# Optimization experiments

Hardware: AMD Instinct MI355X
Metric: run time of the kernel (lower is better)

Reference implementation:

```python
import jax, jax.numpy as jnp
import numpy as np

B, T, C, H = 8, 2048, 1024, 64  # batch, seq (block_size), n_embd, head_size


def setup_inputs() -> dict:
    key = jax.random.key(0)
    kx, kq, kk, kv = jax.random.split(key, 4)
    s = 1.0 / np.sqrt(C)
    return {
        "x": jax.random.normal(kx, (B, T, C), dtype=jnp.float32),
        "Wq": jax.random.normal(kq, (C, H), dtype=jnp.float32) * s,
        "Wk": jax.random.normal(kk, (C, H), dtype=jnp.float32) * s,
        "Wv": jax.random.normal(kv, (C, H), dtype=jnp.float32) * s,
    }


def reference(x, Wq, Wk, Wv):
    t = x.shape[1]
    q = jnp.einsum("btc,ch->bth", x, Wq)
    k = jnp.einsum("btc,ch->bth", x, Wk)
    v = jnp.einsum("btc,ch->bth", x, Wv)
    scores = jnp.einsum("bqh,bkh->bqk", q, k) / jnp.sqrt(jnp.float32(H))
    causal = jnp.tril(jnp.ones((t, t), dtype=bool))  # tril mask
    scores = jnp.where(causal, scores, -jnp.inf)
    attn = jax.nn.softmax(scores, axis=-1)
    return jnp.einsum("bqk,bkh->bqh", attn, v)
```

## Files before the change

### kernel.cpp

```cpp
#include <hip/hip_runtime.h>
#include <hip/hip_bf16.h>

#define BB 8
#define TT 2048
#define CC 1024
#define HH 64
#define NSPLIT 8

typedef __attribute__((ext_vector_type(8)))  short bf16x8;
typedef __attribute__((ext_vector_type(4)))  float f32x4;
typedef __attribute__((ext_vector_type(16))) float f32x16;
typedef __attribute__((ext_vector_type(8)))  unsigned short us8;
typedef __attribute__((ext_vector_type(4)))  unsigned short us4;
typedef unsigned int u32;

static __device__ __forceinline__ unsigned short f2bf(float f) {
    union { float f; unsigned int u; } v; v.f = f;
    unsigned int u = v.u;
    return (unsigned short)((u + 0x7FFFu + ((u >> 16) & 1u)) >> 16);
}
static __device__ __forceinline__ float bf2f(unsigned short s) {
    union { u32 u; float f; } v; v.u = ((u32)s) << 16; return v.f;
}

__global__ __launch_bounds__(256) void prep_weights(
        const float* __restrict__ Wq, const float* __restrict__ Wk,
        const float* __restrict__ Wv, unsigned short* __restrict__ Wt) {
    __shared__ float tile[64][65];
    int w  = blockIdx.x >> 4;
    int c0 = (blockIdx.x & 15) * 64;
    const float* W = (w == 0) ? Wq : (w == 1) ? Wk : Wv;
    int li = threadIdx.x;
    {
        int c = li >> 2, h4 = (li & 3) * 16;
        const float* src = W + (size_t)(c0 + c) * HH + h4;
        #pragma unroll
        for (int i = 0; i < 4; ++i) {
            float4 v4 = *(const float4*)(src + i * 4);
            tile[c][h4 + i*4 + 0] = v4.x; tile[c][h4 + i*4 + 1] = v4.y;
            tile[c][h4 + i*4 + 2] = v4.z; tile[c][h4 + i*4 + 3] = v4.w;
        }
    }
    __syncthreads();
    float scale = (w == 0) ? 0.1803368802f : 1.0f;
    int h = li >> 2, cg = (li & 3) * 16;
    unsigned short* dst = Wt + (size_t)w * HH * CC + (size_t)h * CC + c0 + cg;
    #pragma unroll
    for (int i = 0; i < 16; ++i) dst[i] = f2bf(tile[cg + i][h] * scale);
}

__global__ __launch_bounds__(512, 4) void proj_qkv(
        const float* __restrict__ x, const unsigned short* __restrict__ Wt,
        unsigned short* __restrict__ qws, unsigned short* __restrict__ kws,
        unsigned short* __restrict__ vws) {
    __shared__ unsigned short Xs[2][64 * 64];
    __shared__ unsigned short Ws[2][192 * 64];
    int tid = threadIdx.x;
    int wv = tid >> 6, lane = tid & 63;
    int quad = (lane >> 4) & 3, lq = lane & 15;
    int mg = wv >> 2, ng = wv & 3;
    int r0 = blockIdx.x * 64;

    int xr = tid >> 3, xg = tid & 7;
    const float* xsrc = x + (size_t)(r0 + xr) * CC + xg * 8;
    int xdst = xr * 64 + ((xg ^ (xr & 7)) * 8);
    float4 xa[2], xb[2];

    f32x4 acc[2][3];
    #pragma unroll
    for (int mt = 0; mt < 2; ++mt)
        #pragma unroll
        for (int nt = 0; nt < 3; ++nt)
            #pragma unroll
            for (int i = 0; i < 4; ++i) acc[mt][nt][i] = 0.0f;

    auto stageW = [&](int buf, int kc) {
        #pragma unroll
        for (int i = 0; i < 3; ++i) {
            int fp = tid + i * 512;
            int r = fp >> 3, pb = fp & 7, g = pb ^ (r & 7);
            const u32 __attribute__((address_space(1)))* gsrc =
                (const u32 __attribute__((address_space(1)))*)
                    (Wt + (size_t)r * CC + kc * 64 + g * 8);
            u32 __attribute__((address_space(3)))* ldst =
                (u32 __attribute__((address_space(3)))*)(&Ws[buf][fp * 8]);
            __builtin_amdgcn_global_load_lds(gsrc, ldst, 16, 0, 0);
        }
    };
    auto loadX = [&](int set, int kc) {
        xa[set] = *(const float4*)(xsrc + kc * 64);
        xb[set] = *(const float4*)(xsrc + kc * 64 + 4);
    };
    auto writeX = [&](int set, int buf) {
        unsigned short h[8];
        h[0]=f2bf(xa[set].x); h[1]=f2bf(xa[set].y);
        h[2]=f2bf(xa[set].z); h[3]=f2bf(xa[set].w);
        h[4]=f2bf(xb[set].x); h[5]=f2bf(xb[set].y);
        h[6]=f2bf(xb[set].z); h[7]=f2bf(xb[set].w);
        *(us8*)&Xs[buf][xdst] = *(const us8*)h;
    };

    stageW(0, 0);
    loadX(0, 0); loadX(1, 1);
    writeX(0, 0);

    for (int kc = 0; kc < 16; ++kc) {
        int cur = kc & 1;
        if (kc < 15) asm volatile("s_waitcnt vmcnt(2) lgkmcnt(0)" ::: "memory");
        else         asm volatile("s_waitcnt vmcnt(0) lgkmcnt(0)" ::: "memory");
        __builtin_amdgcn_sched_barrier(0);
        __builtin_amdgcn_s_barrier();
        if (kc < 15) stageW(1 - cur, kc + 1);
        if (kc < 14) loadX(kc & 1, kc + 2);
        #pragma unroll
        for (int ks = 0; ks < 2; ++ks) {
            int g = ks * 4 + quad;
            bf16x8 a[2], b[3];
            #pragma unroll
            for (int mt = 0; mt < 2; ++mt) {
                int arow = mg * 32 + mt * 16 + lq;
                a[mt] = *(const bf16x8*)&Xs[cur][arow * 64 + (g ^ (lq & 7)) * 8];
            }
            #pragma unroll
            for (int nt = 0; nt < 3; ++nt) {
                int brow = ng * 48 + nt * 16 + lq;
                b[nt] = *(const bf16x8*)&Ws[cur][brow * 64 + (g ^ (lq & 7)) * 8];
            }
            #pragma unroll
            for (int mt = 0; mt < 2; ++mt)
                #pragma unroll
                for (int nt = 0; nt < 3; ++nt)
                    acc[mt][nt] = __builtin_amdgcn_mfma_f32_16x16x32_bf16(
                        a[mt], b[nt], acc[mt][nt], 0, 0, 0);
        }
        if (kc < 15) writeX((kc + 1) & 1, 1 - cur);
    }

    int bidx = r0 >> 11;
    int t0base = r0 & (TT - 1);
    #pragma unroll
    for (int mt = 0; mt < 2; ++mt) {
        #pragma unroll
        for (int nt = 0; nt < 3; ++nt) {
            int gcol = ng * 48 + nt * 16 + lq;
            int rloc = mg * 32 + mt * 16 + quad * 4;
            if (gcol < 64) {
                #pragma unroll
                for (int i = 0; i < 4; ++i)
                    qws[(size_t)(r0 + rloc + i) * HH + gcol] =
                        f2bf(acc[mt][nt][i]);
            } else if (gcol < 128) {
                #pragma unroll
                for (int i = 0; i < 4; ++i)
                    kws[(size_t)(r0 + rloc + i) * HH + (gcol - 64)] =
                        f2bf(acc[mt][nt][i]);
            } else {
                unsigned short o[4];
                #pragma unroll
                for (int i = 0; i < 4; ++i) o[i] = f2bf(acc[mt][nt][i]);
                *(us4*)(vws + ((size_t)bidx * HH + (gcol - 128)) * TT
                            + t0base + rloc) = *(const us4*)o;
            }
        }
    }
}

__global__ __launch_bounds__(128, 3) void attn(
        const unsigned short* __restrict__ qws,
        const unsigned short* __restrict__ kws,
        const unsigned short* __restrict__ vws,
        unsigned short* __restrict__ Op, float* __restrict__ Lp) {
    __shared__ unsigned short Kt[32][72];
    __shared__ unsigned short Vt[64][40];
    __shared__ unsigned short Ps[64][40];
    int ti = blockIdx.x;
    int s  = blockIdx.y;
    int b  = blockIdx.z;
    int last = 2 * ti + 1;
    if (s > last) return;
    int tid = threadIdx.x, wv = tid >> 6, lane = tid & 63;
    int half = lane >> 5, l31 = lane & 31;

    bf16x8 qf[4];
    {
        const unsigned short* qp =
            qws + ((size_t)b * TT + ti * 64 + wv * 32 + l31) * HH + half * 8;
        #pragma unroll
        for (int ks = 0; ks < 4; ++ks) qf[ks] = *(const bf16x8*)(qp + ks * 16);
    }
    f32x16 O0, O1, Lc;
    #pragma unroll
    for (int i = 0; i < 16; ++i) { O0[i] = 0.f; O1[i] = 0.f; Lc[i] = 0.f; }
    bf16x8 ones;
    #pragma unroll
    for (int i = 0; i < 8; ++i) ones[i] = (short)0x3F80;

    int kr = tid >> 3, kg = tid & 7;
    int vh = tid >> 2, vkb = tid & 3;
    const unsigned short* ksrc0 = kws + ((size_t)b * TT + kr) * HH + kg * 8;
    const unsigned short* vsrc0 = vws + ((size_t)b * HH + vh) * TT + vkb * 8;

    us8 rk[2], rv[2];
    auto loadKV = [&](int jc) {
        rk[0] = *(const us8*)(ksrc0 + (size_t)(jc * 32) * HH);
        rk[1] = *(const us8*)(ksrc0 + (size_t)(jc * 32 + 16) * HH);
        rv[0] = *(const us8*)(vsrc0 + jc * 32);
        rv[1] = *(const us8*)(vsrc0 + (size_t)32 * TT + jc * 32);
    };
    auto writeKV = [&]() {
        *(us8*)&Kt[kr][kg * 8]       = rk[0];
        *(us8*)&Kt[kr + 16][kg * 8]  = rk[1];
        *(us8*)&Vt[vh][vkb * 8]      = rv[0];
        *(us8*)&Vt[vh + 32][vkb * 8] = rv[1];
    };

    loadKV(s);
    for (int jc = s; jc <= last; jc += NSPLIT) {
        __syncthreads();
        writeKV();
        if (jc + NSPLIT <= last) loadKV(jc + NSPLIT);
        __syncthreads();
        f32x16 S;
        #pragma unroll
        for (int i = 0; i < 16; ++i) S[i] = 0.f;
        #pragma unroll
        for (int ks = 0; ks < 4; ++ks) {
            bf16x8 kf = *(const bf16x8*)&Kt[l31][ks * 16 + half * 8];
            S = __builtin_amdgcn_mfma_f32_32x32x16_bf16(qf[ks], kf, S, 0, 0, 0);
        }
        bool diag = (jc >= 2 * ti + wv);
        #pragma unroll
        for (int r = 0; r < 16; ++r) {
            int pat = (r & 3) + 8 * (r >> 2) + 4 * half;
            float p = __builtin_amdgcn_exp2f(S[r]);
            if (diag && jc * 32 + l31 > ti * 64 + wv * 32 + pat) p = 0.0f;
            Ps[wv * 32 + pat][l31] = f2bf(p);
        }
        #pragma unroll
        for (int ks = 0; ks < 2; ++ks) {
            bf16x8 pa  = *(const bf16x8*)&Ps[wv * 32 + l31][ks * 16 + half * 8];
            bf16x8 vf0 = *(const bf16x8*)&Vt[l31][ks * 16 + half * 8];
            bf16x8 vf1 = *(const bf16x8*)&Vt[32 + l31][ks * 16 + half * 8];
            O0 = __builtin_amdgcn_mfma_f32_32x32x16_bf16(pa, vf0, O0, 0, 0, 0);
            O1 = __builtin_amdgcn_mfma_f32_32x32x16_bf16(pa, vf1, O1, 0, 0, 0);
            Lc = __builtin_amdgcn_mfma_f32_32x32x16_bf16(pa, ones, Lc, 0, 0, 0);
        }
    }
    unsigned short* Ob =
        Op + (((size_t)s * BB + b) * TT + ti * 64 + wv * 32) * HH;
    #pragma unroll
    for (int r = 0; r < 16; ++r) {
        int pat = (r & 3) + 8 * (r >> 2) + 4 * half;
        Ob[(size_t)pat * HH + l31]      = f2bf(O0[r]);
        Ob[(size_t)pat * HH + 32 + l31] = f2bf(O1[r]);
    }
    if (l31 == 0) {
        #pragma unroll
        for (int r = 0; r < 16; ++r) {
            int pat = (r & 3) + 8 * (r >> 2) + 4 * half;
            Lp[((size_t)s * BB + b) * TT + ti * 64 + wv * 32 + pat] = Lc[r];
        }
    }
}

__global__ __launch_bounds__(256) void norm_out(
        const unsigned short* __restrict__ Op, const float* __restrict__ Lp,
        float* __restrict__ out) {
    int idx = blockIdx.x * 256 + threadIdx.x;
    int g = idx >> 2;
    int hseg = (idx & 3) * 16;
    int ti = (g & (TT - 1)) >> 6;
    int ns = min(2 * ti + 2, NSPLIT);
    float a[16];
    #pragma unroll
    for (int j = 0; j < 16; ++j) a[j] = 0.f;
    float Ls = 0.f;
    for (int s = 0; s < ns; ++s) {
        const unsigned short* base =
            Op + ((size_t)s * BB * TT + g) * HH + hseg;
        us8 u0 = *(const us8*)base;
        us8 u1 = *(const us8*)(base + 8);
        #pragma unroll
        for (int j = 0; j < 8; ++j) { a[j] += bf2f(u0[j]); a[8 + j] += bf2f(u1[j]); }
        Ls += Lp[(size_t)s * BB * TT + g];
    }
    float inv = 1.0f / Ls;
    float* ob = out + (size_t)g * HH + hseg;
    #pragma unroll
    for (int q = 0; q < 4; ++q) {
        float4 v = make_float4(a[q*4] * inv, a[q*4+1] * inv,
                               a[q*4+2] * inv, a[q*4+3] * inv);
        ((float4*)ob)[q] = v;
    }
}

extern "C" void kernel_launch(void* const* d_in, const int* in_sizes, int n_in,
                              void* d_out, int out_size, void* d_ws, size_t ws_size,
                              hipStream_t stream) {
    (void)in_sizes; (void)n_in; (void)out_size; (void)ws_size;
    const float* x  = (const float*)d_in[0];
    const float* Wq = (const float*)d_in[1];
    const float* Wk = (const float*)d_in[2];
    const float* Wv = (const float*)d_in[3];
    float* out = (float*)d_out;

    char* ws = (char*)d_ws;
    unsigned short* Wt  = (unsigned short*)ws;
    unsigned short* qws = (unsigned short*)(ws + (1u << 19));
    unsigned short* kws = (unsigned short*)(ws + (1u << 19) + (1u << 21));
    unsigned short* vws = (unsigned short*)(ws + (1u << 19) + (2u << 21));
    unsigned short* Op  = (unsigned short*)(ws + (1u << 19) + (3u << 21));
    float*          Lp  = (float*)(ws + (1u << 19) + (3u << 21) + (1u << 24));

    prep_weights<<<48, 256, 0, stream>>>(Wq, Wk, Wv, Wt);
    proj_qkv<<<256, 512, 0, stream>>>(x, Wt, qws, kws, vws);
    attn<<<dim3(32, NSPLIT, 8), 128, 0, stream>>>(qws, kws, vws, Op, Lp);
    norm_out<<<256, 256, 0, stream>>>(Op, Lp, out);
}
```

Measured before the change: 134.3 us.

## Use 64-wide KV chunks with fewer splits and MFMA priority hints

The attention kernel now processes 64-key chunks per iteration instead of 32, computing two S tiles per wave and doing four PV k-steps. The KV split count drops from 8 to 4, and norm_out's partial count changes to match. s_setprio is raised around the MFMA sections. The aim is fewer barriers and loop iterations per key and less partial-output traffic in the reduction, at the cost of more LDS, lower occupancy (launch bounds 3→2 blocks) and less parallelism per query tile.

```diff
diff --git a/kernel.cpp b/kernel.cpp
--- a/kernel.cpp
+++ b/kernel.cpp
@@ -5,7 +5,7 @@
 #define TT 2048
 #define CC 1024
 #define HH 64
-#define NSPLIT 8
+#define NSPLIT 4
 
 typedef __attribute__((ext_vector_type(8)))  short bf16x8;
 typedef __attribute__((ext_vector_type(4)))  float f32x4;
@@ -165,19 +165,18 @@
     }
 }
 
-__global__ __launch_bounds__(128, 3) void attn(
+__global__ __launch_bounds__(128, 2) void attn(
         const unsigned short* __restrict__ qws,
         const unsigned short* __restrict__ kws,
         const unsigned short* __restrict__ vws,
         unsigned short* __restrict__ Op, float* __restrict__ Lp) {
-    __shared__ unsigned short Kt[32][72];
-    __shared__ unsigned short Vt[64][40];
-    __shared__ unsigned short Ps[64][40];
+    __shared__ unsigned short Kt[64][72];
+    __shared__ unsigned short Vt[64][72];
+    __shared__ unsigned short Ps[64][72];
     int ti = blockIdx.x;
     int s  = blockIdx.y;
     int b  = blockIdx.z;
-    int last = 2 * ti + 1;
-    if (s > last) return;
+    if (s > ti) return;
     int tid = threadIdx.x, wv = tid >> 6, lane = tid & 63;
     int half = lane >> 5, l31 = lane & 31;
 
@@ -195,49 +194,61 @@
     #pragma unroll
     for (int i = 0; i < 8; ++i) ones[i] = (short)0x3F80;
 
-    int kr = tid >> 3, kg = tid & 7;
-    int vh = tid >> 2, vkb = tid & 3;
-    const unsigned short* ksrc0 = kws + ((size_t)b * TT + kr) * HH + kg * 8;
-    const unsigned short* vsrc0 = vws + ((size_t)b * HH + vh) * TT + vkb * 8;
-
-    us8 rk[2], rv[2];
+    int sr = tid >> 3, sg = tid & 7;
+    const unsigned short* ksrc0 = kws + ((size_t)b * TT + sr) * HH + sg * 8;
+    const unsigned short* vsrc0 = vws + ((size_t)b * HH + sr) * TT + sg * 8;
+
+    us8 rk[4], rv[4];
     auto loadKV = [&](int jc) {
-        rk[0] = *(const us8*)(ksrc0 + (size_t)(jc * 32) * HH);
-        rk[1] = *(const us8*)(ksrc0 + (size_t)(jc * 32 + 16) * HH);
-        rv[0] = *(const us8*)(vsrc0 + jc * 32);
-        rv[1] = *(const us8*)(vsrc0 + (size_t)32 * TT + jc * 32);
+        #pragma unroll
+        for (int i = 0; i < 4; ++i)
+            rk[i] = *(const us8*)(ksrc0 + (size_t)(jc * 64 + i * 16) * HH);
+        #pragma unroll
+        for (int i = 0; i < 4; ++i)
+            rv[i] = *(const us8*)(vsrc0 + (size_t)(i * 16) * TT + jc * 64);
     };
     auto writeKV = [&]() {
-        *(us8*)&Kt[kr][kg * 8]       = rk[0];
-        *(us8*)&Kt[kr + 16][kg * 8]  = rk[1];
-        *(us8*)&Vt[vh][vkb * 8]      = rv[0];
-        *(us8*)&Vt[vh + 32][vkb * 8] = rv[1];
+        #pragma unroll
+        for (int i = 0; i < 4; ++i) *(us8*)&Kt[sr + i * 16][sg * 8] = rk[i];
+        #pragma unroll
+        for (int i = 0; i < 4; ++i) *(us8*)&Vt[sr + i * 16][sg * 8] = rv[i];
     };
 
     loadKV(s);
-    for (int jc = s; jc <= last; jc += NSPLIT) {
+    for (int jc = s; jc <= ti; jc += NSPLIT) {
         __syncthreads();
         writeKV();
-        if (jc + NSPLIT <= last) loadKV(jc + NSPLIT);
+        if (jc + NSPLIT <= ti) loadKV(jc + NSPLIT);
         __syncthreads();
-        f32x16 S;
-        #pragma unroll
-        for (int i = 0; i < 16; ++i) S[i] = 0.f;
+        f32x16 S0, S1;
+        #pragma unroll
+        for (int i = 0; i < 16; ++i) { S0[i] = 0.f; S1[i] = 0.f; }
+        __builtin_amdgcn_s_setprio(1);
         #pragma unroll
         for (int ks = 0; ks < 4; ++ks) {
-            bf16x8 kf = *(const bf16x8*)&Kt[l31][ks * 16 + half * 8];
-            S = __builtin_amdgcn_mfma_f32_32x32x16_bf16(qf[ks], kf, S, 0, 0, 0);
-        }
-        bool diag = (jc >= 2 * ti + wv);
+            bf16x8 kf0 = *(const bf16x8*)&Kt[l31][ks * 16 + half * 8];
+            bf16x8 kf1 = *(const bf16x8*)&Kt[32 + l31][ks * 16 + half * 8];
+            S0 = __builtin_amdgcn_mfma_f32_32x32x16_bf16(qf[ks], kf0, S0, 0, 0, 0);
+            S1 = __builtin_amdgcn_mfma_f32_32x32x16_bf16(qf[ks], kf1, S1, 0, 0, 0);
+        }
+        __builtin_amdgcn_s_setprio(0);
+        bool diag = (jc == ti);
         #pragma unroll
         for (int r = 0; r < 16; ++r) {
             int pat = (r & 3) + 8 * (r >> 2) + 4 * half;
-            float p = __builtin_amdgcn_exp2f(S[r]);
-            if (diag && jc * 32 + l31 > ti * 64 + wv * 32 + pat) p = 0.0f;
-            Ps[wv * 32 + pat][l31] = f2bf(p);
-        }
-        #pragma unroll
-        for (int ks = 0; ks < 2; ++ks) {
+            float p0 = __builtin_amdgcn_exp2f(S0[r]);
+            float p1 = __builtin_amdgcn_exp2f(S1[r]);
+            if (diag) {
+                int rloc = wv * 32 + pat;
+                if (l31 > rloc)      p0 = 0.0f;
+                if (32 + l31 > rloc) p1 = 0.0f;
+            }
+            Ps[wv * 32 + pat][l31]      = f2bf(p0);
+            Ps[wv * 32 + pat][32 + l31] = f2bf(p1);
+        }
+        __builtin_amdgcn_s_setprio(1);
+        #pragma unroll
+        for (int ks = 0; ks < 4; ++ks) {
             bf16x8 pa  = *(const bf16x8*)&Ps[wv * 32 + l31][ks * 16 + half * 8];
             bf16x8 vf0 = *(const bf16x8*)&Vt[l31][ks * 16 + half * 8];
             bf16x8 vf1 = *(const bf16x8*)&Vt[32 + l31][ks * 16 + half * 8];
@@ -245,6 +256,7 @@
             O1 = __builtin_amdgcn_mfma_f32_32x32x16_bf16(pa, vf1, O1, 0, 0, 0);
             Lc = __builtin_amdgcn_mfma_f32_32x32x16_bf16(pa, ones, Lc, 0, 0, 0);
         }
+        __builtin_amdgcn_s_setprio(0);
     }
     unsigned short* Ob =
         Op + (((size_t)s * BB + b) * TT + ti * 64 + wv * 32) * HH;
@@ -270,7 +282,7 @@
     int g = idx >> 2;
     int hseg = (idx & 3) * 16;
     int ti = (g & (TT - 1)) >> 6;
-    int ns = min(2 * ti + 2, NSPLIT);
+    int ns = min(ti + 1, NSPLIT);
     float a[16];
     #pragma unroll
     for (int j = 0; j < 16; ++j) a[j] = 0.f;
```

Measured after the change: 131.4 us. -2.2%, faster.
